# Kernel tuning notes

Measured on AMD Instinct MI355X. Metric: run time of the kernel, lower is better.

Reference implementation:

```python
import jax, jax.numpy as jnp
import numpy as np

EMBED_DIM = 1024
NUM_HEADS = 16
HEAD_DIM = EMBED_DIM // NUM_HEADS
SCALE = 1.0 / np.sqrt(HEAD_DIM)


def _quant_linear(x, w, b):
    # Per-tensor symmetric int8 quantize -> dequantize -> GEMM (faithful to QuantizedLinear)
    s = jnp.max(jnp.abs(w)) / 127.0
    w_dq = jnp.clip(jnp.round(w / s), -128.0, 127.0) * s
    return jnp.einsum('bse,oe->bso', x, w_dq) + b


def setup_inputs() -> dict:
    key = jax.random.key(0)
    ks = jax.random.split(key, 7)
    B, S, E = 2, 2048, EMBED_DIM
    return {
        'query': jax.random.normal(ks[0], (B, S, E), dtype=jnp.float32),
        'key': jax.random.normal(ks[1], (B, S, E), dtype=jnp.float32),
        'value': jax.random.normal(ks[2], (B, S, E), dtype=jnp.float32),
        'Wq': jax.random.normal(ks[3], (E, E), dtype=jnp.float32) * 0.02,
        'bq': jnp.zeros((E,), dtype=jnp.float32),
        'Wk': jax.random.normal(ks[4], (E, E), dtype=jnp.float32) * 0.02,
        'bk': jnp.zeros((E,), dtype=jnp.float32),
        'Wv': jax.random.normal(ks[5], (E, E), dtype=jnp.float32) * 0.02,
        'bv': jnp.zeros((E,), dtype=jnp.float32),
        'Wo': jax.random.normal(ks[6], (E, E), dtype=jnp.float32) * 0.02,
        'bo': jnp.zeros((E,), dtype=jnp.float32),
    }


def reference(query, key, value, Wq, bq, Wk, bk, Wv, bv, Wo, bo):
    B, S, E = query.shape
    H, D = NUM_HEADS, HEAD_DIM
    Q = _quant_linear(query, Wq, bq).reshape(B, S, H, D).transpose(0, 2, 1, 3)
    K = _quant_linear(key, Wk, bk).reshape(B, S, H, D).transpose(0, 2, 1, 3)
    V = _quant_linear(value, Wv, bv).reshape(B, S, H, D).transpose(0, 2, 1, 3)
    # [B,H,S,S] unfused attention scores
    scores = jnp.einsum('bhqd,bhkd->bhqk', Q, K) * SCALE
    attn = jax.nn.softmax(scores, axis=-1)  # dropout is identity at inference
    out = jnp.einsum('bhqk,bhkd->bhqd', attn, V)
    out = out.transpose(0, 2, 1, 3).reshape(B, S, E)
    return _quant_linear(out, Wo, bo)
```

## Files before the change

### kernel.cpp

```cpp
#include <hip/hip_runtime.h>
#include <math.h>

#define S_LEN 2048
#define EMB   1024
#define NHEAD 16
#define HDIM  64
#define MTOT  4096
#define EXP2_SCALE 0.18033688011112042f

typedef __attribute__((ext_vector_type(8))) short bf16x8;
typedef __attribute__((ext_vector_type(8))) _Float16 f16x8;
typedef __attribute__((ext_vector_type(4))) float f32x4;

#if __has_builtin(__builtin_amdgcn_exp2f)
#define FEXP2(x) __builtin_amdgcn_exp2f(x)
#else
#define FEXP2(x) exp2f(x)
#endif

__device__ __forceinline__ short f2bf(float f) {
  union { float f; unsigned u; } v; v.f = f;
  unsigned r = v.u + 0x7fffu + ((v.u >> 16) & 1u);
  return (short)(r >> 16);
}
__device__ __forceinline__ float bf2f(short s) {
  union { float f; unsigned u; } v; v.u = ((unsigned)(unsigned short)s) << 16;
  return v.f;
}
__device__ __forceinline__ short f2h(float f) {
  union { _Float16 h; short s; } u; u.h = (_Float16)f; return u.s;
}
__device__ __forceinline__ unsigned pkbf(float e0, float e1) {
  unsigned a = __float_as_uint(e1) + 0x8000u;
  unsigned b = __float_as_uint(e0) + 0x8000u;
  return __builtin_amdgcn_perm(a, b, 0x07060302u);
}

__device__ __forceinline__ void gload_lds16(const void* g, void* l) {
  __builtin_amdgcn_global_load_lds(
      (const __attribute__((address_space(1))) void*)g,
      (__attribute__((address_space(3))) void*)l, 16, 0, 0);
}

__global__ void wabsmax_k(const float* __restrict__ W0, const float* __restrict__ W1,
                          const float* __restrict__ W2, const float* __restrict__ W3,
                          unsigned* __restrict__ scaleU) {
  int w = blockIdx.x & 3;
  int part = blockIdx.x >> 2;
  const float* W = (w == 0) ? W0 : (w == 1) ? W1 : (w == 2) ? W2 : W3;
  float m = 0.f;
  int base = part * 16384;
#pragma unroll
  for (int p = 0; p < 16; ++p) {
    const float4 v = *(const float4*)&W[base + p * 1024 + threadIdx.x * 4];
    m = fmaxf(m, fmaxf(fmaxf(fabsf(v.x), fabsf(v.y)), fmaxf(fabsf(v.z), fabsf(v.w))));
  }
  __shared__ float red[256];
  red[threadIdx.x] = m;
  __syncthreads();
  for (int s = 128; s > 0; s >>= 1) {
    if (threadIdx.x < s) red[threadIdx.x] = fmaxf(red[threadIdx.x], red[threadIdx.x + s]);
    __syncthreads();
  }
  if (threadIdx.x == 0) atomicMax(&scaleU[w], __float_as_uint(red[0]));
}

__global__ void wqa_k(const float* __restrict__ W0, const float* __restrict__ W1,
                      const float* __restrict__ W2, const float* __restrict__ W3,
                      short* __restrict__ Q0, short* __restrict__ Q1,
                      short* __restrict__ Q2, short* __restrict__ Q3,
                      const float* __restrict__ A0, const float* __restrict__ A1,
                      const float* __restrict__ A2,
                      short* __restrict__ H0, short* __restrict__ H1,
                      short* __restrict__ H2,
                      const unsigned* __restrict__ scaleU, float* __restrict__ sVal) {
  int y = blockIdx.y;
  if (y < 4) {
    if (blockIdx.x >= 1024) return;
    const float* W = (y == 0) ? W0 : (y == 1) ? W1 : (y == 2) ? W2 : W3;
    short* Q = (y == 0) ? Q0 : (y == 1) ? Q1 : (y == 2) ? Q2 : Q3;
    float s = __uint_as_float(scaleU[y]) * (1.0f / 127.0f);
    if (blockIdx.x == 0 && threadIdx.x == 0) sVal[y] = s;
    int idx = (blockIdx.x * 256 + threadIdx.x) * 4;
    float4 v = *(const float4*)&W[idx];
    float qx = fminf(fmaxf(rintf(v.x / s), -128.f), 127.f);
    float qy = fminf(fmaxf(rintf(v.y / s), -128.f), 127.f);
    float qz = fminf(fmaxf(rintf(v.z / s), -128.f), 127.f);
    float qw = fminf(fmaxf(rintf(v.w / s), -128.f), 127.f);
    short4 q;
    if (y == 3) { q.x = f2h(qx); q.y = f2h(qy); q.z = f2h(qz); q.w = f2h(qw); }
    else        { q.x = f2bf(qx); q.y = f2bf(qy); q.z = f2bf(qz); q.w = f2bf(qw); }
    *(short4*)&Q[idx] = q;
  } else {
    int w = y - 4;
    const float* A = (w == 0) ? A0 : (w == 1) ? A1 : A2;
    short* H = (w == 0) ? H0 : (w == 1) ? H1 : H2;
    int idx = (blockIdx.x * 256 + threadIdx.x) * 4;
    float4 v = *(const float4*)&A[idx];
    short4 h;
    h.x = f2bf(v.x); h.y = f2bf(v.y); h.z = f2bf(v.z); h.w = f2bf(v.w);
    *(short4*)&H[idx] = h;
  }
}

__device__ __forceinline__ void gemm_core(
    const short* __restrict__ Ah, const short* __restrict__ Bq, int m0, int n0,
    short* AhS, short* BsS, f32x4 acc[4][4]) {
  const int tid = threadIdx.x;
  const int lane = tid & 63, wave = tid >> 6;
  const int quad = lane >> 4, l16 = lane & 15;
  const int wm = wave >> 1, wn = wave & 1;

  const int swrow = lane >> 2, swcol = (lane & 3) * 8;
  const short* agh = Ah + (m0 + wave * 32 + swrow) * 1024 + swcol;
  const short* bgp = Bq + (n0 + wave * 32 + swrow) * 1024 + swcol;
  short* sA0 = AhS + wave * 1024;
  short* sB0 = BsS + wave * 1024;

  for (int k0 = 0; k0 < 1024; k0 += 64) {
    __syncthreads();
    gload_lds16(agh + k0,                  sA0);
    gload_lds16(agh + 16 * 1024 + k0,      sA0 + 512);
    gload_lds16(agh + k0 + 32,             sA0 + 4096);
    gload_lds16(agh + 16 * 1024 + k0 + 32, sA0 + 4096 + 512);
    gload_lds16(bgp + k0,                  sB0);
    gload_lds16(bgp + 16 * 1024 + k0,      sB0 + 512);
    gload_lds16(bgp + k0 + 32,             sB0 + 4096);
    gload_lds16(bgp + 16 * 1024 + k0 + 32, sB0 + 4096 + 512);
    __syncthreads();
    bf16x8 ah[4][2], bb[4][2];
#pragma unroll
    for (int mi = 0; mi < 4; ++mi) {
      int row = wm * 64 + mi * 16 + l16;
      ah[mi][0] = *(const bf16x8*)&AhS[row * 32 + quad * 8];
      ah[mi][1] = *(const bf16x8*)&AhS[4096 + row * 32 + quad * 8];
    }
#pragma unroll
    for (int ni = 0; ni < 4; ++ni) {
      int row = wn * 64 + ni * 16 + l16;
      bb[ni][0] = *(const bf16x8*)&BsS[row * 32 + quad * 8];
      bb[ni][1] = *(const bf16x8*)&BsS[4096 + row * 32 + quad * 8];
    }
#pragma unroll
    for (int mi = 0; mi < 4; ++mi)
#pragma unroll
      for (int ni = 0; ni < 4; ++ni) {
        acc[mi][ni] = __builtin_amdgcn_mfma_f32_16x16x32_bf16(ah[mi][0], bb[ni][0], acc[mi][ni], 0, 0, 0);
        acc[mi][ni] = __builtin_amdgcn_mfma_f32_16x16x32_bf16(ah[mi][1], bb[ni][1], acc[mi][ni], 0, 0, 0);
      }
  }
}

__global__ __launch_bounds__(256, 2) void gemm_qkv(
    const short* __restrict__ QA, const short* __restrict__ KA, const short* __restrict__ VA,
    const short* __restrict__ WqQ, const short* __restrict__ WkQ, const short* __restrict__ WvQ,
    const float* __restrict__ sVal,
    const float* __restrict__ bq, const float* __restrict__ bk, const float* __restrict__ bv,
    short* __restrict__ Qh, short* __restrict__ Kh, short* __restrict__ Vh) {
  __shared__ __align__(16) short AhS[2 * 128 * 32];
  __shared__ __align__(16) short BsS[2 * 128 * 32];
  const int z = blockIdx.z;
  const short* Ah = (z == 0) ? QA : (z == 1) ? KA : VA;
  const short* Bq = (z == 0) ? WqQ : (z == 1) ? WkQ : WvQ;
  const float* bias = (z == 0) ? bq : (z == 1) ? bk : bv;
  short* oh = (z == 0) ? Qh : (z == 1) ? Kh : Vh;

  const int lin = blockIdx.y * 8 + blockIdx.x;
  const int map = (lin & 7) * 32 + (lin >> 3);
  const int m0 = (map >> 3) * 128, n0 = (map & 7) * 128;
  f32x4 acc[4][4];
#pragma unroll
  for (int i = 0; i < 4; ++i)
#pragma unroll
    for (int j = 0; j < 4; ++j) acc[i][j] = (f32x4){0.f, 0.f, 0.f, 0.f};

  gemm_core(Ah, Bq, m0, n0, AhS, BsS, acc);

  const int lane = threadIdx.x & 63, wave = threadIdx.x >> 6;
  const int quad = lane >> 4, l16 = lane & 15;
  const int wm = wave >> 1, wn = wave & 1;
  float s = sVal[z];
  float post = (z == 0) ? EXP2_SCALE : 1.0f;
#pragma unroll
  for (int mi = 0; mi < 4; ++mi) {
#pragma unroll
    for (int ni = 0; ni < 4; ++ni) {
      int rowb = m0 + wm * 64 + mi * 16 + quad * 4;
      int col = n0 + wn * 64 + ni * 16 + l16;
      float bia = bias[col];
      int h = col >> 6, d = col & 63;
      if (z < 2) {
#pragma unroll
        for (int r = 0; r < 4; ++r) {
          float v = (acc[mi][ni][r] * s + bia) * post;
          int row = rowb + r;
          int b = row >> 11, sq = row & 2047;
          oh[((b * 16 + h) * 2048 + sq) * 64 + d] = f2bf(v);
        }
      } else {
        int b = rowb >> 11, sq = rowb & 2047;
        short4 pk;
        pk.x = f2bf(acc[mi][ni][0] * s + bia);
        pk.y = f2bf(acc[mi][ni][1] * s + bia);
        pk.z = f2bf(acc[mi][ni][2] * s + bia);
        pk.w = f2bf(acc[mi][ni][3] * s + bia);
        *(short4*)&oh[((b * 16 + h) * 64 + d) * 2048 + sq] = pk;
      }
    }
  }
}

__global__ __launch_bounds__(256, 2) void gemm_o(
    const short* __restrict__ OA, const short* __restrict__ WoQ,
    const float* __restrict__ sPtr, const float* __restrict__ bias,
    float* __restrict__ outF) {
  __shared__ __align__(16) short AhS[2 * 128 * 32];
  __shared__ __align__(16) short BsS[2 * 64 * 32];
  const int tid = threadIdx.x;
  const int lane = tid & 63, wave = tid >> 6;
  const int quad = lane >> 4, l16 = lane & 15;
  const int lin = blockIdx.y * 16 + blockIdx.x;
  const int map = (lin & 7) * 64 + (lin >> 3);
  const int m0 = (map >> 4) * 128, n0 = (map & 15) * 64;

  f32x4 acc[2][4];
#pragma unroll
  for (int i = 0; i < 2; ++i)
#pragma unroll
    for (int j = 0; j < 4; ++j) acc[i][j] = (f32x4){0.f, 0.f, 0.f, 0.f};

  const int swrow = lane >> 2, swcol = (lane & 3) * 8;
  const short* agh = OA + (m0 + wave * 32 + swrow) * 1024 + swcol;
  const short* bgp = WoQ + (n0 + wave * 16 + swrow) * 1024 + swcol;
  short* sA0 = AhS + wave * 1024;
  short* sB0 = BsS + wave * 512;

  for (int k0 = 0; k0 < 1024; k0 += 64) {
    __syncthreads();
    gload_lds16(agh + k0,                  sA0);
    gload_lds16(agh + 16 * 1024 + k0,      sA0 + 512);
    gload_lds16(agh + k0 + 32,             sA0 + 4096);
    gload_lds16(agh + 16 * 1024 + k0 + 32, sA0 + 4096 + 512);
    gload_lds16(bgp + k0,                  sB0);
    gload_lds16(bgp + k0 + 32,             sB0 + 2048);
    __syncthreads();
    f16x8 ah[2][2], bb[4][2];
#pragma unroll
    for (int mi = 0; mi < 2; ++mi) {
      int row = wave * 32 + mi * 16 + l16;
      ah[mi][0] = *(const f16x8*)&AhS[row * 32 + quad * 8];
      ah[mi][1] = *(const f16x8*)&AhS[4096 + row * 32 + quad * 8];
    }
#pragma unroll
    for (int ni = 0; ni < 4; ++ni) {
      int row = ni * 16 + l16;
      bb[ni][0] = *(const f16x8*)&BsS[row * 32 + quad * 8];
      bb[ni][1] = *(const f16x8*)&BsS[2048 + row * 32 + quad * 8];
    }
#pragma unroll
    for (int mi = 0; mi < 2; ++mi)
#pragma unroll
      for (int ni = 0; ni < 4; ++ni) {
        acc[mi][ni] = __builtin_amdgcn_mfma_f32_16x16x32_f16(ah[mi][0], bb[ni][0], acc[mi][ni], 0, 0, 0);
        acc[mi][ni] = __builtin_amdgcn_mfma_f32_16x16x32_f16(ah[mi][1], bb[ni][1], acc[mi][ni], 0, 0, 0);
      }
  }

  const float s = *sPtr;
#pragma unroll
  for (int mi = 0; mi < 2; ++mi) {
#pragma unroll
    for (int ni = 0; ni < 4; ++ni) {
      int rowb = m0 + wave * 32 + mi * 16 + quad * 4;
      int col = n0 + ni * 16 + l16;
      float bia = bias[col];
#pragma unroll
      for (int r = 0; r < 4; ++r)
        outF[(rowb + r) * 1024 + col] = acc[mi][ni][r] * s + bia;
    }
  }
}

__global__ __launch_bounds__(256, 2) void flash_k(
    const short* __restrict__ Qh, const short* __restrict__ Kh,
    const short* __restrict__ Vh,
    short* __restrict__ Oh) {
  __shared__ __align__(16) short Khs[64 * 72];
  __shared__ __align__(16) short Vhs[64 * 72];

  const int tid = threadIdx.x;
  const int lane = tid & 63, wave = tid >> 6;
  const int quad = lane >> 4, l16 = lane & 15;
  const int bh = blockIdx.y;
  const int b = bh >> 4, h = bh & 15;
  const int q0 = blockIdx.x * 128 + wave * 32;
  const int qkbase = bh * (S_LEN * HDIM);
  const int vbase  = bh * (HDIM * S_LEN);

  bf16x8 qb[2][2];
#pragma unroll
  for (int g = 0; g < 2; ++g) {
    const int qrow = qkbase + (q0 + g * 16 + l16) * HDIM;
    qb[g][0] = *(const bf16x8*)&Qh[qrow + quad * 8];
    qb[g][1] = *(const bf16x8*)&Qh[qrow + 32 + quad * 8];
  }

  f32x4 zero = {0.f, 0.f, 0.f, 0.f};
  f32x4 oacc[2][4];
#pragma unroll
  for (int g = 0; g < 2; ++g)
#pragma unroll
    for (int i = 0; i < 4; ++i) oacc[g][i] = zero;
  f32x4 sacc[2] = {zero, zero};

  union { bf16x8 v; unsigned u[4]; } ones_;
  ones_.u[0] = ones_.u[1] = ones_.u[2] = ones_.u[3] = 0x3F803F80u;

  const int sr  = wave * 16 + l16;
  const int sc8 = quad * 8;
  const int srP = (sr & 32) | (((sr >> 2) & 1) << 4) | (((sr >> 3) & 3) << 2) | (sr & 3);
  const int kgl = qkbase + sr * HDIM + sc8;
  const int vgl = vbase + sr * S_LEN + sc8;
  const int kOff = srP * 72 + sc8;
  const int vOff = sr * 72 + sc8;

  bf16x8 pk0 = *(const bf16x8*)&Kh[kgl];
  bf16x8 pk1 = *(const bf16x8*)&Kh[kgl + 32];
  bf16x8 pv0 = *(const bf16x8*)&Vh[vgl];
  bf16x8 pv1 = *(const bf16x8*)&Vh[vgl + 32];

  for (int kt = 0; kt < S_LEN; kt += 64) {
    __syncthreads();
    *(bf16x8*)&Khs[kOff]      = pk0;
    *(bf16x8*)&Khs[kOff + 32] = pk1;
    *(bf16x8*)&Vhs[vOff]      = pv0;
    *(bf16x8*)&Vhs[vOff + 32] = pv1;
    __syncthreads();
    if (kt + 64 < S_LEN) {
      int kg = kgl + (kt + 64) * HDIM;
      int vg = vgl + (kt + 64);
      pk0 = *(const bf16x8*)&Kh[kg];
      pk1 = *(const bf16x8*)&Kh[kg + 32];
      pv0 = *(const bf16x8*)&Vh[vg];
      pv1 = *(const bf16x8*)&Vh[vg + 32];
    }
    __builtin_amdgcn_s_setprio(1);
    f32x4 sc[2][4];
#pragma unroll
    for (int nj = 0; nj < 4; ++nj) {
      const int kr = nj * 16 + l16;
      bf16x8 kf0 = *(const bf16x8*)&Khs[kr * 72 + quad * 8];
      bf16x8 kf1 = *(const bf16x8*)&Khs[kr * 72 + 32 + quad * 8];
#pragma unroll
      for (int g = 0; g < 2; ++g) {
        f32x4 sv = zero;
        sv = __builtin_amdgcn_mfma_f32_16x16x32_bf16(kf0, qb[g][0], sv, 0, 0, 0);
        sv = __builtin_amdgcn_mfma_f32_16x16x32_bf16(kf1, qb[g][1], sv, 0, 0, 0);
        sc[g][nj] = sv;
      }
    }
    __builtin_amdgcn_s_setprio(0);
#pragma unroll
    for (int g = 0; g < 2; ++g)
#pragma unroll
      for (int nj = 0; nj < 4; ++nj)
#pragma unroll
        for (int r = 0; r < 4; ++r)
          sc[g][nj][r] = FEXP2(sc[g][nj][r]);
    union { bf16x8 v; unsigned u[4]; } P[2][2];
#pragma unroll
    for (int g = 0; g < 2; ++g) {
      P[g][0].u[0] = pkbf(sc[g][0][0], sc[g][0][1]);
      P[g][0].u[1] = pkbf(sc[g][0][2], sc[g][0][3]);
      P[g][0].u[2] = pkbf(sc[g][1][0], sc[g][1][1]);
      P[g][0].u[3] = pkbf(sc[g][1][2], sc[g][1][3]);
      P[g][1].u[0] = pkbf(sc[g][2][0], sc[g][2][1]);
      P[g][1].u[1] = pkbf(sc[g][2][2], sc[g][2][3]);
      P[g][1].u[2] = pkbf(sc[g][3][0], sc[g][3][1]);
      P[g][1].u[3] = pkbf(sc[g][3][2], sc[g][3][3]);
    }
    __builtin_amdgcn_s_setprio(1);
#pragma unroll
    for (int g = 0; g < 2; ++g) {
      sacc[g] = __builtin_amdgcn_mfma_f32_16x16x32_bf16(P[g][0].v, ones_.v, sacc[g], 0, 0, 0);
      sacc[g] = __builtin_amdgcn_mfma_f32_16x16x32_bf16(P[g][1].v, ones_.v, sacc[g], 0, 0, 0);
    }
#pragma unroll
    for (int ni = 0; ni < 4; ++ni) {
      int vr = ni * 16 + l16;
      bf16x8 vf0 = *(const bf16x8*)&Vhs[vr * 72 + quad * 8];
      bf16x8 vf1 = *(const bf16x8*)&Vhs[vr * 72 + 32 + quad * 8];
#pragma unroll
      for (int g = 0; g < 2; ++g) {
        oacc[g][ni] = __builtin_amdgcn_mfma_f32_16x16x32_bf16(P[g][0].v, vf0, oacc[g][ni], 0, 0, 0);
        oacc[g][ni] = __builtin_amdgcn_mfma_f32_16x16x32_bf16(P[g][1].v, vf1, oacc[g][ni], 0, 0, 0);
      }
    }
    __builtin_amdgcn_s_setprio(0);
  }
#pragma unroll
  for (int g = 0; g < 2; ++g) {
#pragma unroll
    for (int r = 0; r < 4; ++r) {
      float inv = 1.f / sacc[g][r];
      int row = b * S_LEN + q0 + g * 16 + quad * 4 + r;
#pragma unroll
      for (int ni = 0; ni < 4; ++ni) {
        float v = oacc[g][ni][r] * inv;
        int idx = row * 1024 + h * 64 + ni * 16 + l16;
        Oh[idx] = f2h(v);
      }
    }
  }
}

extern "C" void kernel_launch(void* const* d_in, const int* in_sizes, int n_in,
                              void* d_out, int out_size, void* d_ws, size_t ws_size,
                              hipStream_t stream) {
  const float* query = (const float*)d_in[0];
  const float* key_i = (const float*)d_in[1];
  const float* value = (const float*)d_in[2];
  const float* Wq = (const float*)d_in[3];
  const float* bq = (const float*)d_in[4];
  const float* Wk = (const float*)d_in[5];
  const float* bk = (const float*)d_in[6];
  const float* Wv = (const float*)d_in[7];
  const float* bv = (const float*)d_in[8];
  const float* Wo = (const float*)d_in[9];
  const float* bo = (const float*)d_in[10];
  float* out = (float*)d_out;

  char* w = (char*)d_ws;
  unsigned* scaleU = (unsigned*)w;
  float* sVal = (float*)(w + 256);
  size_t off = 512;
  const size_t SZ_W = 2097152;
  const size_t SZ_A = 8388608;
  short* WqQ = (short*)(w + off); off += SZ_W;
  short* WkQ = (short*)(w + off); off += SZ_W;
  short* WvQ = (short*)(w + off); off += SZ_W;
  short* WoQ = (short*)(w + off); off += SZ_W;
  short* Qa  = (short*)(w + off); off += SZ_A;
  short* Ka  = (short*)(w + off); off += SZ_A;
  short* Va  = (short*)(w + off); off += SZ_A;
  short* Qh  = (short*)(w + off); off += SZ_A;
  short* Kh  = (short*)(w + off); off += SZ_A;
  short* Vh  = (short*)(w + off); off += SZ_A;
  short* Oh  = Qa;

  (void)hipMemsetAsync(scaleU, 0, 16, stream);
  wabsmax_k<<<256, 256, 0, stream>>>(Wq, Wk, Wv, Wo, scaleU);
  wqa_k<<<dim3(4096, 7), 256, 0, stream>>>(Wq, Wk, Wv, Wo, WqQ, WkQ, WvQ, WoQ,
                                           query, key_i, value, Qa, Ka, Va,
                                           scaleU, sVal);
  gemm_qkv<<<dim3(8, 32, 3), 256, 0, stream>>>(Qa, Ka, Va, WqQ, WkQ, WvQ, sVal,
                                               bq, bk, bv, Qh, Kh, Vh);
  flash_k<<<dim3(16, 32), 256, 0, stream>>>(Qh, Kh, Vh, Oh);
  gemm_o<<<dim3(16, 32), 256, 0, stream>>>(Oh, WoQ, sVal + 3, bo, out);
}
```

Measured before the change: 224.2 us.

## Fuse fp32-to-bf16 activation conversion into QKV GEMM A-tile loading

Drops the separate pass that converted the query, key and value activations to bf16 in workspace buffers. The QKV GEMM now reads fp32 activations directly into registers, prefetching one k-step ahead, then packs them to bf16 and writes them to LDS itself. This removes a full write and reread of 24 MB of intermediate activations and shrinks the pre-pass kernel to weight quantization only. In exchange the A path uses register-staged loads instead of direct global-to-LDS loads, and each tile reads twice as many bytes in fp32, which raises register pressure.

After: 218.9 us. 2.4% less time.

```diff
diff --git a/kernel.cpp b/kernel.cpp
--- a/kernel.cpp
+++ b/kernel.cpp
@@ -65,94 +65,40 @@
   if (threadIdx.x == 0) atomicMax(&scaleU[w], __float_as_uint(red[0]));
 }
 
-__global__ void wqa_k(const float* __restrict__ W0, const float* __restrict__ W1,
-                      const float* __restrict__ W2, const float* __restrict__ W3,
-                      short* __restrict__ Q0, short* __restrict__ Q1,
-                      short* __restrict__ Q2, short* __restrict__ Q3,
-                      const float* __restrict__ A0, const float* __restrict__ A1,
-                      const float* __restrict__ A2,
-                      short* __restrict__ H0, short* __restrict__ H1,
-                      short* __restrict__ H2,
-                      const unsigned* __restrict__ scaleU, float* __restrict__ sVal) {
-  int y = blockIdx.y;
-  if (y < 4) {
-    if (blockIdx.x >= 1024) return;
-    const float* W = (y == 0) ? W0 : (y == 1) ? W1 : (y == 2) ? W2 : W3;
-    short* Q = (y == 0) ? Q0 : (y == 1) ? Q1 : (y == 2) ? Q2 : Q3;
-    float s = __uint_as_float(scaleU[y]) * (1.0f / 127.0f);
-    if (blockIdx.x == 0 && threadIdx.x == 0) sVal[y] = s;
-    int idx = (blockIdx.x * 256 + threadIdx.x) * 4;
-    float4 v = *(const float4*)&W[idx];
-    float qx = fminf(fmaxf(rintf(v.x / s), -128.f), 127.f);
-    float qy = fminf(fmaxf(rintf(v.y / s), -128.f), 127.f);
-    float qz = fminf(fmaxf(rintf(v.z / s), -128.f), 127.f);
-    float qw = fminf(fmaxf(rintf(v.w / s), -128.f), 127.f);
-    short4 q;
-    if (y == 3) { q.x = f2h(qx); q.y = f2h(qy); q.z = f2h(qz); q.w = f2h(qw); }
-    else        { q.x = f2bf(qx); q.y = f2bf(qy); q.z = f2bf(qz); q.w = f2bf(qw); }
-    *(short4*)&Q[idx] = q;
-  } else {
-    int w = y - 4;
-    const float* A = (w == 0) ? A0 : (w == 1) ? A1 : A2;
-    short* H = (w == 0) ? H0 : (w == 1) ? H1 : H2;
-    int idx = (blockIdx.x * 256 + threadIdx.x) * 4;
-    float4 v = *(const float4*)&A[idx];
-    short4 h;
-    h.x = f2bf(v.x); h.y = f2bf(v.y); h.z = f2bf(v.z); h.w = f2bf(v.w);
-    *(short4*)&H[idx] = h;
-  }
-}
-
-__device__ __forceinline__ void gemm_core(
-    const short* __restrict__ Ah, const short* __restrict__ Bq, int m0, int n0,
-    short* AhS, short* BsS, f32x4 acc[4][4]) {
-  const int tid = threadIdx.x;
-  const int lane = tid & 63, wave = tid >> 6;
-  const int quad = lane >> 4, l16 = lane & 15;
-  const int wm = wave >> 1, wn = wave & 1;
-
-  const int swrow = lane >> 2, swcol = (lane & 3) * 8;
-  const short* agh = Ah + (m0 + wave * 32 + swrow) * 1024 + swcol;
-  const short* bgp = Bq + (n0 + wave * 32 + swrow) * 1024 + swcol;
-  short* sA0 = AhS + wave * 1024;
-  short* sB0 = BsS + wave * 1024;
-
-  for (int k0 = 0; k0 < 1024; k0 += 64) {
-    __syncthreads();
-    gload_lds16(agh + k0,                  sA0);
-    gload_lds16(agh + 16 * 1024 + k0,      sA0 + 512);
-    gload_lds16(agh + k0 + 32,             sA0 + 4096);
-    gload_lds16(agh + 16 * 1024 + k0 + 32, sA0 + 4096 + 512);
-    gload_lds16(bgp + k0,                  sB0);
-    gload_lds16(bgp + 16 * 1024 + k0,      sB0 + 512);
-    gload_lds16(bgp + k0 + 32,             sB0 + 4096);
-    gload_lds16(bgp + 16 * 1024 + k0 + 32, sB0 + 4096 + 512);
-    __syncthreads();
-    bf16x8 ah[4][2], bb[4][2];
-#pragma unroll
-    for (int mi = 0; mi < 4; ++mi) {
-      int row = wm * 64 + mi * 16 + l16;
-      ah[mi][0] = *(const bf16x8*)&AhS[row * 32 + quad * 8];
-      ah[mi][1] = *(const bf16x8*)&AhS[4096 + row * 32 + quad * 8];
-    }
-#pragma unroll
-    for (int ni = 0; ni < 4; ++ni) {
-      int row = wn * 64 + ni * 16 + l16;
-      bb[ni][0] = *(const bf16x8*)&BsS[row * 32 + quad * 8];
-      bb[ni][1] = *(const bf16x8*)&BsS[4096 + row * 32 + quad * 8];
-    }
-#pragma unroll
-    for (int mi = 0; mi < 4; ++mi)
-#pragma unroll
-      for (int ni = 0; ni < 4; ++ni) {
-        acc[mi][ni] = __builtin_amdgcn_mfma_f32_16x16x32_bf16(ah[mi][0], bb[ni][0], acc[mi][ni], 0, 0, 0);
-        acc[mi][ni] = __builtin_amdgcn_mfma_f32_16x16x32_bf16(ah[mi][1], bb[ni][1], acc[mi][ni], 0, 0, 0);
-      }
-  }
-}
+__global__ void wquant_k(const float* __restrict__ W0, const float* __restrict__ W1,
+                         const float* __restrict__ W2, const float* __restrict__ W3,
+                         short* __restrict__ Q0, short* __restrict__ Q1,
+                         short* __restrict__ Q2, short* __restrict__ Q3,
+                         const unsigned* __restrict__ scaleU, float* __restrict__ sVal) {
+  int w = blockIdx.y;
+  const float* W = (w == 0) ? W0 : (w == 1) ? W1 : (w == 2) ? W2 : W3;
+  short* Q = (w == 0) ? Q0 : (w == 1) ? Q1 : (w == 2) ? Q2 : Q3;
+  float s = __uint_as_float(scaleU[w]) * (1.0f / 127.0f);
+  if (blockIdx.x == 0 && threadIdx.x == 0) sVal[w] = s;
+  int idx = (blockIdx.x * 256 + threadIdx.x) * 4;
+  float4 v = *(const float4*)&W[idx];
+  float qx = fminf(fmaxf(rintf(v.x / s), -128.f), 127.f);
+  float qy = fminf(fmaxf(rintf(v.y / s), -128.f), 127.f);
+  float qz = fminf(fmaxf(rintf(v.z / s), -128.f), 127.f);
+  float qw = fminf(fmaxf(rintf(v.w / s), -128.f), 127.f);
+  short4 q;
+  if (w == 3) { q.x = f2h(qx); q.y = f2h(qy); q.z = f2h(qz); q.w = f2h(qw); }
+  else        { q.x = f2bf(qx); q.y = f2bf(qy); q.z = f2bf(qz); q.w = f2bf(qw); }
+  *(short4*)&Q[idx] = q;
+}
+
+#define QKV_ALOAD(k0v)                                                        \
+  pa0 = *(const float4*)&aga[(k0v)];                                          \
+  pa1 = *(const float4*)&aga[(k0v) + 4];                                      \
+  pa2 = *(const float4*)&aga[16384 + (k0v)];                                  \
+  pa3 = *(const float4*)&aga[16384 + (k0v) + 4];                              \
+  pa4 = *(const float4*)&aga[(k0v) + 32];                                     \
+  pa5 = *(const float4*)&aga[(k0v) + 36];                                     \
+  pa6 = *(const float4*)&aga[16384 + (k0v) + 32];                             \
+  pa7 = *(const float4*)&aga[16384 + (k0v) + 36];
 
 __global__ __launch_bounds__(256, 2) void gemm_qkv(
-    const short* __restrict__ QA, const short* __restrict__ KA, const short* __restrict__ VA,
+    const float* __restrict__ QA, const float* __restrict__ KA, const float* __restrict__ VA,
     const short* __restrict__ WqQ, const short* __restrict__ WkQ, const short* __restrict__ WvQ,
     const float* __restrict__ sVal,
     const float* __restrict__ bq, const float* __restrict__ bk, const float* __restrict__ bv,
@@ -160,7 +106,7 @@
   __shared__ __align__(16) short AhS[2 * 128 * 32];
   __shared__ __align__(16) short BsS[2 * 128 * 32];
   const int z = blockIdx.z;
-  const short* Ah = (z == 0) ? QA : (z == 1) ? KA : VA;
+  const float* Af = (z == 0) ? QA : (z == 1) ? KA : VA;
   const short* Bq = (z == 0) ? WqQ : (z == 1) ? WkQ : WvQ;
   const float* bias = (z == 0) ? bq : (z == 1) ? bk : bv;
   short* oh = (z == 0) ? Qh : (z == 1) ? Kh : Vh;
@@ -168,17 +114,70 @@
   const int lin = blockIdx.y * 8 + blockIdx.x;
   const int map = (lin & 7) * 32 + (lin >> 3);
   const int m0 = (map >> 3) * 128, n0 = (map & 7) * 128;
-  f32x4 acc[4][4];
-#pragma unroll
-  for (int i = 0; i < 4; ++i)
-#pragma unroll
-    for (int j = 0; j < 4; ++j) acc[i][j] = (f32x4){0.f, 0.f, 0.f, 0.f};
-
-  gemm_core(Ah, Bq, m0, n0, AhS, BsS, acc);
-
-  const int lane = threadIdx.x & 63, wave = threadIdx.x >> 6;
+
+  const int tid = threadIdx.x;
+  const int lane = tid & 63, wave = tid >> 6;
   const int quad = lane >> 4, l16 = lane & 15;
   const int wm = wave >> 1, wn = wave & 1;
+  const int swrow = lane >> 2, swcol = (lane & 3) * 8;
+
+  const float* aga = Af + (m0 + wave * 32 + swrow) * 1024 + swcol;
+  const short* bgp = Bq + (n0 + wave * 32 + swrow) * 1024 + swcol;
+  short* sA0 = AhS + wave * 1024 + lane * 8;
+  short* sB0 = BsS + wave * 1024;
+
+  f32x4 acc[4][4];
+#pragma unroll
+  for (int i = 0; i < 4; ++i)
+#pragma unroll
+    for (int j = 0; j < 4; ++j) acc[i][j] = (f32x4){0.f, 0.f, 0.f, 0.f};
+
+  float4 pa0, pa1, pa2, pa3, pa4, pa5, pa6, pa7;
+  QKV_ALOAD(0)
+
+  for (int k0 = 0; k0 < 1024; k0 += 64) {
+    __syncthreads();
+    union { bf16x8 v; unsigned u[4]; } c;
+    c.u[0] = pkbf(pa0.x, pa0.y); c.u[1] = pkbf(pa0.z, pa0.w);
+    c.u[2] = pkbf(pa1.x, pa1.y); c.u[3] = pkbf(pa1.z, pa1.w);
+    *(bf16x8*)&sA0[0] = c.v;
+    c.u[0] = pkbf(pa2.x, pa2.y); c.u[1] = pkbf(pa2.z, pa2.w);
+    c.u[2] = pkbf(pa3.x, pa3.y); c.u[3] = pkbf(pa3.z, pa3.w);
+    *(bf16x8*)&sA0[512] = c.v;
+    c.u[0] = pkbf(pa4.x, pa4.y); c.u[1] = pkbf(pa4.z, pa4.w);
+    c.u[2] = pkbf(pa5.x, pa5.y); c.u[3] = pkbf(pa5.z, pa5.w);
+    *(bf16x8*)&sA0[4096] = c.v;
+    c.u[0] = pkbf(pa6.x, pa6.y); c.u[1] = pkbf(pa6.z, pa6.w);
+    c.u[2] = pkbf(pa7.x, pa7.y); c.u[3] = pkbf(pa7.z, pa7.w);
+    *(bf16x8*)&sA0[4096 + 512] = c.v;
+    gload_lds16(bgp + k0,                  sB0);
+    gload_lds16(bgp + 16 * 1024 + k0,      sB0 + 512);
+    gload_lds16(bgp + k0 + 32,             sB0 + 4096);
+    gload_lds16(bgp + 16 * 1024 + k0 + 32, sB0 + 4096 + 512);
+    __syncthreads();
+    if (k0 + 64 < 1024) { QKV_ALOAD(k0 + 64) }
+    bf16x8 ah[4][2], bb[4][2];
+#pragma unroll
+    for (int mi = 0; mi < 4; ++mi) {
+      int row = wm * 64 + mi * 16 + l16;
+      ah[mi][0] = *(const bf16x8*)&AhS[row * 32 + quad * 8];
+      ah[mi][1] = *(const bf16x8*)&AhS[4096 + row * 32 + quad * 8];
+    }
+#pragma unroll
+    for (int ni = 0; ni < 4; ++ni) {
+      int row = wn * 64 + ni * 16 + l16;
+      bb[ni][0] = *(const bf16x8*)&BsS[row * 32 + quad * 8];
+      bb[ni][1] = *(const bf16x8*)&BsS[4096 + row * 32 + quad * 8];
+    }
+#pragma unroll
+    for (int mi = 0; mi < 4; ++mi)
+#pragma unroll
+      for (int ni = 0; ni < 4; ++ni) {
+        acc[mi][ni] = __builtin_amdgcn_mfma_f32_16x16x32_bf16(ah[mi][0], bb[ni][0], acc[mi][ni], 0, 0, 0);
+        acc[mi][ni] = __builtin_amdgcn_mfma_f32_16x16x32_bf16(ah[mi][1], bb[ni][1], acc[mi][ni], 0, 0, 0);
+      }
+  }
+
   float s = sVal[z];
   float post = (z == 0) ? EXP2_SCALE : 1.0f;
 #pragma unroll
@@ -440,20 +439,17 @@
   short* WkQ = (short*)(w + off); off += SZ_W;
   short* WvQ = (short*)(w + off); off += SZ_W;
   short* WoQ = (short*)(w + off); off += SZ_W;
-  short* Qa  = (short*)(w + off); off += SZ_A;
-  short* Ka  = (short*)(w + off); off += SZ_A;
-  short* Va  = (short*)(w + off); off += SZ_A;
   short* Qh  = (short*)(w + off); off += SZ_A;
   short* Kh  = (short*)(w + off); off += SZ_A;
   short* Vh  = (short*)(w + off); off += SZ_A;
-  short* Oh  = Qa;
+  short* Oh  = (short*)(w + off); off += SZ_A;
 
   (void)hipMemsetAsync(scaleU, 0, 16, stream);
   wabsmax_k<<<256, 256, 0, stream>>>(Wq, Wk, Wv, Wo, scaleU);
-  wqa_k<<<dim3(4096, 7), 256, 0, stream>>>(Wq, Wk, Wv, Wo, WqQ, WkQ, WvQ, WoQ,
-                                           query, key_i, value, Qa, Ka, Va,
-                                           scaleU, sVal);
-  gemm_qkv<<<dim3(8, 32, 3), 256, 0, stream>>>(Qa, Ka, Va, WqQ, WkQ, WvQ, sVal,
+  wquant_k<<<dim3(1024, 4), 256, 0, stream>>>(Wq, Wk, Wv, Wo, WqQ, WkQ, WvQ, WoQ,
+                                              scaleU, sVal);
+  gemm_qkv<<<dim3(8, 32, 3), 256, 0, stream>>>(query, key_i, value,
+                                               WqQ, WkQ, WvQ, sVal,
                                                bq, bk, bv, Qh, Kh, Vh);
   flash_k<<<dim3(16, 32), 256, 0, stream>>>(Qh, Kh, Vh, Oh);
   gemm_o<<<dim3(16, 32), 256, 0, stream>>>(Oh, WoQ, sVal + 3, bo, out);
```
